# Optimization experiments

Measured on AMD Instinct MI355X. Metric: run time of the kernel, lower is better.

The kernel has to match this reference:

```python
import jax, jax.numpy as jnp
import numpy as np

N = 50000
E = 800000
EPS = 1e-5

def _gcn_conv(x, src, dst, norm, W, b):
    # PyG GCNConv: linear transform, normalized gather/scatter, then bias.
    xw = x @ W                                   # [N, out]
    msgs = xw[src] * norm[:, None]               # [E+N, out] gather
    out = jax.ops.segment_sum(msgs, dst, num_segments=N)  # scatter-add
    return out + b

def _bn_eval(x, gamma, beta, mean, var):
    return (x - mean) * jax.lax.rsqrt(var + EPS) * gamma + beta

def setup_inputs() -> dict:
    key = jax.random.key(0)
    ks = jax.random.split(key, 24)
    dims = [(128, 256), (256, 128), (128, 64), (64, 6)]
    inp = {
        "x": jax.random.normal(ks[0], (N, 128), dtype=jnp.float32),
        "edge_index": jax.random.randint(ks[1], (2, E), 0, N, dtype=jnp.int64),
    }
    i = 2
    for li, (fi, fo) in enumerate(dims, start=1):
        scale = 1.0 / np.sqrt(fi)
        inp[f"W{li}"] = jax.random.uniform(ks[i], (fi, fo), jnp.float32, -scale, scale); i += 1
        inp[f"b{li}"] = jnp.zeros((fo,), jnp.float32)
        if li < 4:  # BN after first three convs
            inp[f"g{li}"] = jnp.ones((fo,), jnp.float32)
            inp[f"be{li}"] = jnp.zeros((fo,), jnp.float32)
            inp[f"m{li}"] = 0.1 * jax.random.normal(ks[i], (fo,), jnp.float32); i += 1
            inp[f"v{li}"] = jax.random.uniform(ks[i], (fo,), jnp.float32, 0.5, 1.5); i += 1
    return inp

def reference(x, edge_index,
              W1, b1, g1, be1, m1, v1,
              W2, b2, g2, be2, m2, v2,
              W3, b3, g3, be3, m3, v3,
              W4, b4):
    # Add self-loops once; symmetric normalization deg^-1/2 (with self-loops).
    loops = jnp.arange(N, dtype=edge_index.dtype)
    src = jnp.concatenate([edge_index[0], loops])
    dst = jnp.concatenate([edge_index[1], loops])
    deg = jax.ops.segment_sum(jnp.ones_like(dst, dtype=x.dtype), dst, num_segments=N)
    dinv = jnp.where(deg > 0, jax.lax.rsqrt(deg), 0.0)
    norm = dinv[src] * dinv[dst]  # [E+N]

    h = _gcn_conv(x, src, dst, norm, W1, b1)
    h = jax.nn.relu(_bn_eval(h, g1, be1, m1, v1))  # dropout: no-op in eval
    h = _gcn_conv(h, src, dst, norm, W2, b2)
    h = jax.nn.relu(_bn_eval(h, g2, be2, m2, v2))
    h = _gcn_conv(h, src, dst, norm, W3, b3)
    h = jax.nn.relu(_bn_eval(h, g3, be3, m3, v3))
    return _gcn_conv(h, src, dst, norm, W4, b4)
```

## Files before the change

### kernel.cpp

```cpp
#include <hip/hip_runtime.h>
#include <hip/hip_bf16.h>
#include <hip/hip_fp16.h>

#define EPS 1e-5f

constexpr int NN = 50000;
constexpr int NE = 800000;

typedef __attribute__((ext_vector_type(8))) __bf16 bf16x8;
typedef __attribute__((ext_vector_type(4))) float f32x4;

__global__ void memset_i32(int* p, int n) {
  int i = blockIdx.x * blockDim.x + threadIdx.x;
  if (i < n) p[i] = 0;
}

__global__ void deg_kernel(const int* __restrict__ dst, int* __restrict__ degi, int n) {
  int i = blockIdx.x * blockDim.x + threadIdx.x;
  if (i < n) atomicAdd(&degi[dst[i]], 1);
}

__global__ __launch_bounds__(1024) void scan1(const int* __restrict__ cnt,
                                              int* __restrict__ incl,
                                              int* __restrict__ bsum, int n) {
  __shared__ int s[1024];
  int tid = threadIdx.x;
  int i = blockIdx.x * 1024 + tid;
  int v = (i < n) ? cnt[i] : 0;
  s[tid] = v;
  __syncthreads();
  for (int off = 1; off < 1024; off <<= 1) {
    int t = (tid >= off) ? s[tid - off] : 0;
    __syncthreads();
    s[tid] += t;
    __syncthreads();
  }
  if (i < n) incl[i] = s[tid];
  if (tid == 1023) bsum[blockIdx.x] = s[1023];
}

__global__ void scan2(int* __restrict__ bsum, int nb) {
  int lane = threadIdx.x;
  int v = (lane < nb) ? bsum[lane] : 0;
  int orig = v;
  for (int off = 1; off < 64; off <<= 1) {
    int t = __shfl_up(v, off, 64);
    if (lane >= off) v += t;
  }
  if (lane < nb) bsum[lane] = v - orig;
}

__global__ __launch_bounds__(1024) void scan3(const int* __restrict__ cnt,
                                              const int* __restrict__ incl,
                                              const int* __restrict__ bsum,
                                              int* __restrict__ rp,
                                              int* __restrict__ cursor,
                                              float* __restrict__ dinv, int n) {
  int tid = threadIdx.x;
  int i = blockIdx.x * 1024 + tid;
  if (i < n) {
    int v = incl[i] + bsum[blockIdx.x];
    rp[i + 1] = v;
    cursor[i] = v - cnt[i];
    dinv[i] = rsqrtf((float)(cnt[i] + 1));
  }
  if (i == 0) rp[0] = 0;
}

__global__ void fill_kernel(const int* __restrict__ src, const int* __restrict__ dst,
                            int* __restrict__ cursor, unsigned short* __restrict__ col,
                            int n) {
  int i = blockIdx.x * blockDim.x + threadIdx.x;
  if (i < n) {
    int pos = atomicAdd(&cursor[dst[i]], 1);
    col[pos] = (unsigned short)src[i];
  }
}

__device__ __forceinline__ void wsplit_one(const float* W, __bf16* th, __bf16* tl,
                                           int j, int K, int N) {
  int k = j / N, n = j - k * N;
  float v = W[j];
  __bf16 h = (__bf16)v;
  th[(size_t)n * K + k] = h;
  tl[(size_t)n * K + k] = (__bf16)(v - (float)h);
}

__global__ void wsplit_all(const float* __restrict__ W1, __bf16* t1h, __bf16* t1l,
                           const float* __restrict__ W2, __bf16* t2h, __bf16* t2l,
                           const float* __restrict__ W3, __bf16* t3h, __bf16* t3l,
                           const float* __restrict__ W4, __bf16* t4h, __bf16* t4l) {
  int i = blockIdx.x * blockDim.x + threadIdx.x;
  if (i < 32768) wsplit_one(W1, t1h, t1l, i, 128, 256);
  else if (i < 65536) wsplit_one(W2, t2h, t2l, i - 32768, 256, 128);
  else if (i < 73728) wsplit_one(W3, t3h, t3l, i - 65536, 128, 64);
  else if (i < 74112) wsplit_one(W4, t4h, t4l, i - 73728, 64, 6);
}

__global__ void scale_half(const float* __restrict__ x, const float* __restrict__ dinv,
                           __half* __restrict__ o, int n4) {
  int i = blockIdx.x * blockDim.x + threadIdx.x;
  if (i >= n4) return;
  int v = i >> 5;
  float4 t = ((const float4*)x)[i];
  float s = dinv[v];
  __half2 a = __floats2half2_rn(t.x * s, t.y * s);
  __half2 b = __floats2half2_rn(t.z * s, t.w * s);
  __half2* o2 = (__half2*)o;
  o2[i * 2] = a;
  o2[i * 2 + 1] = b;
}

template <int F, int EPI>
__global__ __launch_bounds__(256, 8) void prop_half(
    const __half* __restrict__ in, const int* __restrict__ rp,
    const unsigned short* __restrict__ col,
    const float* __restrict__ dinv, const float* __restrict__ bias,
    const float* __restrict__ gam, const float* __restrict__ bet,
    const float* __restrict__ mean, const float* __restrict__ var,
    __bf16* __restrict__ out_hi, __bf16* __restrict__ out_lo, int nnodes) {
  int tid = threadIdx.x;
  int wid = tid >> 6, lane = tid & 63;
  constexpr int VEC = F / 64;
  int v = blockIdx.x * 4 + wid;
  if (v >= nnodes) return;
  int e0 = rp[v], e1 = rp[v + 1];
  float acc[VEC];
  if constexpr (VEC == 2) {
    float2 f = __half22float2(*(const __half2*)(in + (size_t)v * F + lane * 2));
    acc[0] = f.x; acc[1] = f.y;
  } else {
    acc[0] = __half2float(in[(size_t)v * F + lane]);
  }
  int e1m1 = e1 - 1;
  constexpr int D = 8;
  for (int e = e0; e < e1; e += D) {
    int ss[D];
    float w[D];
    bool full = (e + D <= e1);
    if (full) {
#pragma unroll
      for (int u = 0; u < D; u++) { ss[u] = col[e + u]; w[u] = 1.f; }
    } else {
#pragma unroll
      for (int u = 0; u < D; u++) {
        int ei = e + u;
        ss[u] = col[ei < e1m1 ? ei : e1m1];
        w[u] = (ei < e1) ? 1.f : 0.f;
      }
    }
    if constexpr (VEC == 2) {
      __half2 hv[D];
#pragma unroll
      for (int u = 0; u < D; u++)
        hv[u] = *(const __half2*)(in + (size_t)ss[u] * F + lane * 2);
#pragma unroll
      for (int u = 0; u < D; u++) {
        float2 f = __half22float2(hv[u]);
        acc[0] = fmaf(f.x, w[u], acc[0]);
        acc[1] = fmaf(f.y, w[u], acc[1]);
      }
    } else {
      __half hv[D];
#pragma unroll
      for (int u = 0; u < D; u++) hv[u] = in[(size_t)ss[u] * F + lane];
#pragma unroll
      for (int u = 0; u < D; u++) acc[0] = fmaf(__half2float(hv[u]), w[u], acc[0]);
    }
  }
  float dv = dinv[v];
#pragma unroll
  for (int j = 0; j < VEC; j++) {
    int f = lane * VEC + j;
    float t = acc[j] * dv;
    if constexpr (EPI >= 1) {
      t += bias[f];
      t = (t - mean[f]) * rsqrtf(var[f] + EPS) * gam[f] + bet[f];
      t = fmaxf(t, 0.f);
    }
    __bf16 h = (__bf16)t;
    out_hi[(size_t)v * F + f] = h;
    out_lo[(size_t)v * F + f] = (__bf16)(t - (float)h);
  }
}

__global__ __launch_bounds__(256, 8) void prop_small(
    const float* __restrict__ in, const int* __restrict__ rp,
    const unsigned short* __restrict__ col,
    const float* __restrict__ dinv, const float* __restrict__ bias,
    float* __restrict__ out, int nnodes) {
  constexpr int F = 6;
  int tid = threadIdx.x;
  int wid = tid >> 6, lane = tid & 63;
  int g = lane >> 3, f = lane & 7;
  int v = (blockIdx.x * 4 + wid) * 8 + g;
  if (v >= nnodes || f >= F) return;
  int e0 = rp[v], e1 = rp[v + 1];
  float acc = in[(size_t)v * F + f];
  int e1m1 = e1 - 1;
  constexpr int D = 8;
  for (int e = e0; e < e1; e += D) {
    int ss[D];
    float w[D];
#pragma unroll
    for (int u = 0; u < D; u++) {
      int ei = e + u;
      ss[u] = col[ei < e1m1 ? ei : e1m1];
      w[u] = (ei < e1) ? 1.0f : 0.0f;
    }
#pragma unroll
    for (int u = 0; u < D; u++) acc = fmaf(in[(size_t)ss[u] * F + f], w[u], acc);
  }
  out[(size_t)v * F + f] = acc * dinv[v] + bias[f];
}

template <int BN, int EPI>
__global__ __launch_bounds__(256, 4) void mfma_gemm(
    const __bf16* __restrict__ Ahi, const __bf16* __restrict__ Alo,
    const __bf16* __restrict__ Bhi, const __bf16* __restrict__ Blo,
    const float* __restrict__ bias, const float* __restrict__ gam,
    const float* __restrict__ bet, const float* __restrict__ mean,
    const float* __restrict__ var, const float* __restrict__ dinv,
    float* __restrict__ Cf, __half* __restrict__ Ch,
    __bf16* __restrict__ Chi, __bf16* __restrict__ Clo,
    int M, int K, int N) {
  constexpr int BM = 128, BK = 32, NB = BN / 16;
  __shared__ __bf16 Ah[BM][BK + 8], Al[BM][BK + 8];
  __shared__ __bf16 Bh[BN][BK + 8], Bl[BN][BK + 8];
  int tid = threadIdx.x;
  int wid = tid >> 6, lane = tid & 63;
  int lr = lane & 15, lg = lane >> 4;
  int bm = blockIdx.x * BM, bn = blockIdx.y * BN;
  f32x4 acc[2][NB] = {};
  for (int k0 = 0; k0 < K; k0 += BK) {
#pragma unroll
    for (int c = 0; c < 2; c++) {
      int idx = tid + c * 256;
      int r = idx >> 2, s = idx & 3;
      int rg = bm + r;
      uint4 vh = {0, 0, 0, 0}, vl = {0, 0, 0, 0};
      if (rg < M) {
        size_t go = (size_t)rg * K + k0 + s * 8;
        vh = *reinterpret_cast<const uint4*>(Ahi + go);
        vl = *reinterpret_cast<const uint4*>(Alo + go);
      }
      *reinterpret_cast<uint4*>(&Ah[r][s * 8]) = vh;
      *reinterpret_cast<uint4*>(&Al[r][s * 8]) = vl;
    }
#pragma unroll
    for (int c = 0; c < (BN * 4 + 255) / 256; c++) {
      int idx = tid + c * 256;
      if (idx < BN * 4) {
        int r = idx >> 2, s = idx & 3;
        int rg = bn + r;
        uint4 vh = {0, 0, 0, 0}, vl = {0, 0, 0, 0};
        if (rg < N) {
          size_t go = (size_t)rg * K + k0 + s * 8;
          vh = *reinterpret_cast<const uint4*>(Bhi + go);
          vl = *reinterpret_cast<const uint4*>(Blo + go);
        }
        *reinterpret_cast<uint4*>(&Bh[r][s * 8]) = vh;
        *reinterpret_cast<uint4*>(&Bl[r][s * 8]) = vl;
      }
    }
    __syncthreads();
    int ar = wid * 32 + lr;
    bf16x8 ah0 = *reinterpret_cast<const bf16x8*>(&Ah[ar][lg * 8]);
    bf16x8 ah1 = *reinterpret_cast<const bf16x8*>(&Ah[ar + 16][lg * 8]);
    bf16x8 al0 = *reinterpret_cast<const bf16x8*>(&Al[ar][lg * 8]);
    bf16x8 al1 = *reinterpret_cast<const bf16x8*>(&Al[ar + 16][lg * 8]);
#pragma unroll
    for (int n = 0; n < NB; n++) {
      bf16x8 bh = *reinterpret_cast<const bf16x8*>(&Bh[n * 16 + lr][lg * 8]);
      bf16x8 bl = *reinterpret_cast<const bf16x8*>(&Bl[n * 16 + lr][lg * 8]);
      acc[0][n] = __builtin_amdgcn_mfma_f32_16x16x32_bf16(ah0, bh, acc[0][n], 0, 0, 0);
      acc[1][n] = __builtin_amdgcn_mfma_f32_16x16x32_bf16(ah1, bh, acc[1][n], 0, 0, 0);
      acc[0][n] = __builtin_amdgcn_mfma_f32_16x16x32_bf16(ah0, bl, acc[0][n], 0, 0, 0);
      acc[1][n] = __builtin_amdgcn_mfma_f32_16x16x32_bf16(ah1, bl, acc[1][n], 0, 0, 0);
      acc[0][n] = __builtin_amdgcn_mfma_f32_16x16x32_bf16(al0, bh, acc[0][n], 0, 0, 0);
      acc[1][n] = __builtin_amdgcn_mfma_f32_16x16x32_bf16(al1, bh, acc[1][n], 0, 0, 0);
    }
    __syncthreads();
  }
#pragma unroll
  for (int m = 0; m < 2; m++) {
    int row0 = bm + wid * 32 + m * 16 + lg * 4;
#pragma unroll
    for (int n = 0; n < NB; n++) {
      int colg = bn + n * 16 + lr;
#pragma unroll
      for (int r = 0; r < 4; r++) {
        int row = row0 + r;
        if (row >= M) continue;
        float t = acc[m][n][r];
        if constexpr (EPI == 0) {
          t += bias[colg];
          t = (t - mean[colg]) * rsqrtf(var[colg] + EPS) * gam[colg] + bet[colg];
          t = fmaxf(t, 0.f);
          __bf16 h = (__bf16)t;
          Chi[(size_t)row * N + colg] = h;
          Clo[(size_t)row * N + colg] = (__bf16)(t - (float)h);
        } else if constexpr (EPI == 1) {
          Ch[(size_t)row * N + colg] = __float2half(t * dinv[row]);
        } else {
          if (colg < N) Cf[(size_t)row * N + colg] = t * dinv[row];
        }
      }
    }
  }
}

extern "C" void kernel_launch(void* const* d_in, const int* in_sizes, int n_in,
                              void* d_out, int out_size, void* d_ws, size_t ws_size,
                              hipStream_t stream) {
  const float* x = (const float*)d_in[0];
  const int* ei = (const int*)d_in[1];
  const int* esrc = ei;
  const int* edst = ei + NE;
  const float* W1 = (const float*)d_in[2];  const float* b1 = (const float*)d_in[3];
  const float* g1 = (const float*)d_in[4];  const float* be1 = (const float*)d_in[5];
  const float* m1 = (const float*)d_in[6];  const float* v1 = (const float*)d_in[7];
  const float* W2 = (const float*)d_in[8];  const float* b2 = (const float*)d_in[9];
  const float* g2 = (const float*)d_in[10]; const float* be2 = (const float*)d_in[11];
  const float* m2 = (const float*)d_in[12]; const float* v2 = (const float*)d_in[13];
  const float* W3 = (const float*)d_in[14]; const float* b3 = (const float*)d_in[15];
  const float* g3 = (const float*)d_in[16]; const float* be3 = (const float*)d_in[17];
  const float* m3 = (const float*)d_in[18]; const float* v3 = (const float*)d_in[19];
  const float* W4 = (const float*)d_in[20]; const float* b4 = (const float*)d_in[21];
  float* out = (float*)d_out;

  char* base = (char*)d_ws;
  size_t off = 0;
  auto alloc = [&](size_t bytes) {
    void* p = base + off;
    off = (off + bytes + 255) & ~(size_t)255;
    return p;
  };
  __half* Xh = (__half*)alloc((size_t)NN * 128 * 2);
  float* F1 = (float*)alloc((size_t)NN * 6 * 4);
  __bf16* PAh = (__bf16*)alloc((size_t)NN * 128 * 2);
  __bf16* PAl = (__bf16*)alloc((size_t)NN * 128 * 2);
  __bf16* PHh = (__bf16*)alloc((size_t)NN * 256 * 2);
  __bf16* PHl = (__bf16*)alloc((size_t)NN * 256 * 2);
  __bf16* Wt1h = (__bf16*)alloc(128 * 256 * 2); __bf16* Wt1l = (__bf16*)alloc(128 * 256 * 2);
  __bf16* Wt2h = (__bf16*)alloc(256 * 128 * 2); __bf16* Wt2l = (__bf16*)alloc(256 * 128 * 2);
  __bf16* Wt3h = (__bf16*)alloc(128 * 64 * 2);  __bf16* Wt3l = (__bf16*)alloc(128 * 64 * 2);
  __bf16* Wt4h = (__bf16*)alloc(64 * 6 * 2);    __bf16* Wt4l = (__bf16*)alloc(64 * 6 * 2);
  int* degi = (int*)alloc((size_t)NN * 4);
  float* dinv = (float*)alloc((size_t)NN * 4);
  int* rp = (int*)alloc((size_t)(NN + 1) * 4);
  int* cursor = (int*)alloc((size_t)NN * 4);
  int* incl = (int*)alloc((size_t)NN * 4);
  int* bsum = (int*)alloc(64 * 4);
  unsigned short* col = (unsigned short*)alloc((size_t)NE * 2);

  const int nBlkN = (NN + 255) / 256;
  const int nBlkE = (NE + 255) / 256;
  const int nBlkScan = (NN + 1023) / 1024;
  const int gM = (NN + 127) / 128;
  const int gP = (NN + 3) / 4;

  memset_i32<<<nBlkN, 256, 0, stream>>>(degi, NN);
  deg_kernel<<<nBlkE, 256, 0, stream>>>(edst, degi, NE);
  scan1<<<nBlkScan, 1024, 0, stream>>>(degi, incl, bsum, NN);
  scan2<<<1, 64, 0, stream>>>(bsum, nBlkScan);
  scan3<<<nBlkScan, 1024, 0, stream>>>(degi, incl, bsum, rp, cursor, dinv, NN);
  fill_kernel<<<nBlkE, 256, 0, stream>>>(esrc, edst, cursor, col, NE);

  wsplit_all<<<(74112 + 255) / 256, 256, 0, stream>>>(W1, Wt1h, Wt1l, W2, Wt2h, Wt2l,
                                                      W3, Wt3h, Wt3l, W4, Wt4h, Wt4l);

  scale_half<<<(NN * 32 + 255) / 256, 256, 0, stream>>>(x, dinv, Xh, NN * 32);
  prop_half<128, 0><<<gP, 256, 0, stream>>>(Xh, rp, col, dinv, nullptr, nullptr, nullptr,
                                            nullptr, nullptr, PAh, PAl, NN);
  {
    dim3 g(gM, 2);
    mfma_gemm<128, 0><<<g, 256, 0, stream>>>(PAh, PAl, Wt1h, Wt1l, b1, g1, be1, m1, v1,
                                             nullptr, nullptr, nullptr, PHh, PHl,
                                             NN, 128, 256);
  }
  {
    dim3 g(gM, 1);
    mfma_gemm<128, 1><<<g, 256, 0, stream>>>(PHh, PHl, Wt2h, Wt2l, nullptr, nullptr,
                                             nullptr, nullptr, nullptr, dinv,
                                             nullptr, Xh, nullptr, nullptr, NN, 256, 128);
  }
  prop_half<128, 1><<<gP, 256, 0, stream>>>(Xh, rp, col, dinv, b2, g2, be2, m2, v2,
                                            PAh, PAl, NN);
  {
    dim3 g(gM, 1);
    mfma_gemm<64, 1><<<g, 256, 0, stream>>>(PAh, PAl, Wt3h, Wt3l, nullptr, nullptr,
                                            nullptr, nullptr, nullptr, dinv,
                                            nullptr, Xh, nullptr, nullptr, NN, 128, 64);
  }
  prop_half<64, 1><<<gP, 256, 0, stream>>>(Xh, rp, col, dinv, b3, g3, be3, m3, v3,
                                           PHh, PHl, NN);
  {
    dim3 g(gM, 1);
    mfma_gemm<16, 2><<<g, 256, 0, stream>>>(PHh, PHl, Wt4h, Wt4l, nullptr, nullptr,
                                            nullptr, nullptr, nullptr, dinv,
                                            F1, nullptr, nullptr, nullptr, NN, 64, 6);
  }
  prop_small<<<(NN + 31) / 32, 256, 0, stream>>>(F1, rp, col, dinv, b4, out, NN);
}
```

Before: 287.6 us.

## Partition propagation features into 32-wide column slabs and precompute CSR slot positions

Stores the fp16 propagation input as 32-column slabs (slab-major, node-minor), so each block gathers neighbor rows from a single slab that is small enough to stay cached. Inside a wave, four edge slots of 16 lanes each process edges in parallel and are combined with shuffles. Block indices are interleaved so that blocks working on different slabs of the same nodes run close together in time. CSR construction now records each edge's slot from the degree atomic as a byte, which removes the cursor array and the second atomic pass, and the weight split is merged with the input scaling. This adds reduction overhead, and storing the slot in a byte assumes no node has more than 255 incoming edges.

Result: slower. 355.8 us (+23.7%).

```diff
diff --git a/kernel.cpp b/kernel.cpp
--- a/kernel.cpp
+++ b/kernel.cpp
@@ -8,16 +8,13 @@
 constexpr int NE = 800000;
 
 typedef __attribute__((ext_vector_type(8))) __bf16 bf16x8;
+typedef __attribute__((ext_vector_type(2))) __bf16 bf16x2;
 typedef __attribute__((ext_vector_type(4))) float f32x4;
 
-__global__ void memset_i32(int* p, int n) {
+__global__ void deg_pos(const int* __restrict__ dst, int* __restrict__ degi,
+                        unsigned char* __restrict__ pos8, int n) {
   int i = blockIdx.x * blockDim.x + threadIdx.x;
-  if (i < n) p[i] = 0;
-}
-
-__global__ void deg_kernel(const int* __restrict__ dst, int* __restrict__ degi, int n) {
-  int i = blockIdx.x * blockDim.x + threadIdx.x;
-  if (i < n) atomicAdd(&degi[dst[i]], 1);
+  if (i < n) pos8[i] = (unsigned char)atomicAdd(&degi[dst[i]], 1);
 }
 
 __global__ __launch_bounds__(1024) void scan1(const int* __restrict__ cnt,
@@ -54,27 +51,22 @@
                                               const int* __restrict__ incl,
                                               const int* __restrict__ bsum,
                                               int* __restrict__ rp,
-                                              int* __restrict__ cursor,
                                               float* __restrict__ dinv, int n) {
   int tid = threadIdx.x;
   int i = blockIdx.x * 1024 + tid;
   if (i < n) {
-    int v = incl[i] + bsum[blockIdx.x];
-    rp[i + 1] = v;
-    cursor[i] = v - cnt[i];
+    rp[i + 1] = incl[i] + bsum[blockIdx.x];
     dinv[i] = rsqrtf((float)(cnt[i] + 1));
   }
   if (i == 0) rp[0] = 0;
 }
 
 __global__ void fill_kernel(const int* __restrict__ src, const int* __restrict__ dst,
-                            int* __restrict__ cursor, unsigned short* __restrict__ col,
-                            int n) {
+                            const int* __restrict__ rp,
+                            const unsigned char* __restrict__ pos8,
+                            unsigned short* __restrict__ col, int n) {
   int i = blockIdx.x * blockDim.x + threadIdx.x;
-  if (i < n) {
-    int pos = atomicAdd(&cursor[dst[i]], 1);
-    col[pos] = (unsigned short)src[i];
-  }
+  if (i < n) col[rp[dst[i]] + pos8[i]] = (unsigned short)src[i];
 }
 
 __device__ __forceinline__ void wsplit_one(const float* W, __bf16* th, __bf16* tl,
@@ -86,101 +78,99 @@
   tl[(size_t)n * K + k] = (__bf16)(v - (float)h);
 }
 
-__global__ void wsplit_all(const float* __restrict__ W1, __bf16* t1h, __bf16* t1l,
-                           const float* __restrict__ W2, __bf16* t2h, __bf16* t2l,
-                           const float* __restrict__ W3, __bf16* t3h, __bf16* t3l,
-                           const float* __restrict__ W4, __bf16* t4h, __bf16* t4l) {
+__global__ void wsplit_scale(const float* __restrict__ W1, __bf16* t1h, __bf16* t1l,
+                             const float* __restrict__ W2, __bf16* t2h, __bf16* t2l,
+                             const float* __restrict__ W3, __bf16* t3h, __bf16* t3l,
+                             const float* __restrict__ W4, __bf16* t4h, __bf16* t4l,
+                             const float* __restrict__ x, const float* __restrict__ dinv,
+                             __half* __restrict__ Xq) {
   int i = blockIdx.x * blockDim.x + threadIdx.x;
-  if (i < 32768) wsplit_one(W1, t1h, t1l, i, 128, 256);
-  else if (i < 65536) wsplit_one(W2, t2h, t2l, i - 32768, 256, 128);
-  else if (i < 73728) wsplit_one(W3, t3h, t3l, i - 65536, 128, 64);
-  else if (i < 74112) wsplit_one(W4, t4h, t4l, i - 73728, 64, 6);
-}
-
-__global__ void scale_half(const float* __restrict__ x, const float* __restrict__ dinv,
-                           __half* __restrict__ o, int n4) {
-  int i = blockIdx.x * blockDim.x + threadIdx.x;
-  if (i >= n4) return;
-  int v = i >> 5;
-  float4 t = ((const float4*)x)[i];
+  if (i < 32768) { wsplit_one(W1, t1h, t1l, i, 128, 256); return; }
+  if (i < 65536) { wsplit_one(W2, t2h, t2l, i - 32768, 256, 128); return; }
+  if (i < 73728) { wsplit_one(W3, t3h, t3l, i - 65536, 128, 64); return; }
+  if (i < 74112) { wsplit_one(W4, t4h, t4l, i - 73728, 64, 6); return; }
+  int k = i - 74112;
+  if (k >= NN * 32) return;
+  int v = k >> 5, f = (k & 31) * 4;
+  int q = f >> 5, off = f & 31;
+  float4 t = ((const float4*)x)[k];
   float s = dinv[v];
   __half2 a = __floats2half2_rn(t.x * s, t.y * s);
   __half2 b = __floats2half2_rn(t.z * s, t.w * s);
-  __half2* o2 = (__half2*)o;
-  o2[i * 2] = a;
-  o2[i * 2 + 1] = b;
+  __half2* d = (__half2*)(Xq + ((size_t)q * NN + v) * 32 + off);
+  d[0] = a;
+  d[1] = b;
 }
 
 template <int F, int EPI>
-__global__ __launch_bounds__(256, 8) void prop_half(
-    const __half* __restrict__ in, const int* __restrict__ rp,
+__global__ __launch_bounds__(256, 8) void prop_q(
+    const __half* __restrict__ Xq, const int* __restrict__ rp,
     const unsigned short* __restrict__ col,
     const float* __restrict__ dinv, const float* __restrict__ bias,
     const float* __restrict__ gam, const float* __restrict__ bet,
     const float* __restrict__ mean, const float* __restrict__ var,
     __bf16* __restrict__ out_hi, __bf16* __restrict__ out_lo, int nnodes) {
-  int tid = threadIdx.x;
-  int wid = tid >> 6, lane = tid & 63;
-  constexpr int VEC = F / 64;
-  int v = blockIdx.x * 4 + wid;
+  constexpr int NQ = F / 32;
+  int bid = blockIdx.x;
+  int q, gi;
+  if constexpr (NQ == 4) {
+    q = (bid & 7) >> 1;
+    gi = (bid >> 3) * 2 + (bid & 1);
+  } else {
+    q = (bid & 7) >> 2;
+    gi = (bid >> 3) * 4 + (bid & 3);
+  }
+  int tid = threadIdx.x, wid = tid >> 6, lane = tid & 63;
+  int j = lane & 15, slot = lane >> 4;
+  int v = gi * 4 + wid;
   if (v >= nnodes) return;
+  const __half* X = Xq + (size_t)q * nnodes * 32;
   int e0 = rp[v], e1 = rp[v + 1];
-  float acc[VEC];
-  if constexpr (VEC == 2) {
-    float2 f = __half22float2(*(const __half2*)(in + (size_t)v * F + lane * 2));
-    acc[0] = f.x; acc[1] = f.y;
-  } else {
-    acc[0] = __half2float(in[(size_t)v * F + lane]);
+  float ax = 0.f, ay = 0.f;
+  if (slot == 0) {
+    float2 s = __half22float2(*(const __half2*)(X + (size_t)v * 32 + j * 2));
+    ax = s.x;
+    ay = s.y;
   }
   int e1m1 = e1 - 1;
-  constexpr int D = 8;
-  for (int e = e0; e < e1; e += D) {
-    int ss[D];
-    float w[D];
-    bool full = (e + D <= e1);
-    if (full) {
-#pragma unroll
-      for (int u = 0; u < D; u++) { ss[u] = col[e + u]; w[u] = 1.f; }
-    } else {
-#pragma unroll
-      for (int u = 0; u < D; u++) {
-        int ei = e + u;
-        ss[u] = col[ei < e1m1 ? ei : e1m1];
-        w[u] = (ei < e1) ? 1.f : 0.f;
-      }
-    }
-    if constexpr (VEC == 2) {
-      __half2 hv[D];
-#pragma unroll
-      for (int u = 0; u < D; u++)
-        hv[u] = *(const __half2*)(in + (size_t)ss[u] * F + lane * 2);
-#pragma unroll
-      for (int u = 0; u < D; u++) {
-        float2 f = __half22float2(hv[u]);
-        acc[0] = fmaf(f.x, w[u], acc[0]);
-        acc[1] = fmaf(f.y, w[u], acc[1]);
-      }
-    } else {
-      __half hv[D];
-#pragma unroll
-      for (int u = 0; u < D; u++) hv[u] = in[(size_t)ss[u] * F + lane];
-#pragma unroll
-      for (int u = 0; u < D; u++) acc[0] = fmaf(__half2float(hv[u]), w[u], acc[0]);
-    }
-  }
-  float dv = dinv[v];
-#pragma unroll
-  for (int j = 0; j < VEC; j++) {
-    int f = lane * VEC + j;
-    float t = acc[j] * dv;
+  for (int e = e0; e < e1; e += 16) {
+    int ss[4];
+    float w[4];
+#pragma unroll
+    for (int u = 0; u < 4; u++) {
+      int ei = e + u * 4 + slot;
+      ss[u] = col[ei < e1 ? ei : e1m1];
+      w[u] = (ei < e1) ? 1.f : 0.f;
+    }
+    float2 fv[4];
+#pragma unroll
+    for (int u = 0; u < 4; u++)
+      fv[u] = __half22float2(*(const __half2*)(X + (size_t)ss[u] * 32 + j * 2));
+#pragma unroll
+    for (int u = 0; u < 4; u++) {
+      ax = fmaf(fv[u].x, w[u], ax);
+      ay = fmaf(fv[u].y, w[u], ay);
+    }
+  }
+  ax += __shfl_xor(ax, 16); ax += __shfl_xor(ax, 32);
+  ay += __shfl_xor(ay, 16); ay += __shfl_xor(ay, 32);
+  if (slot == 0) {
+    float dv = dinv[v];
+    int f0 = q * 32 + j * 2;
+    float t0 = ax * dv, t1 = ay * dv;
     if constexpr (EPI >= 1) {
-      t += bias[f];
-      t = (t - mean[f]) * rsqrtf(var[f] + EPS) * gam[f] + bet[f];
-      t = fmaxf(t, 0.f);
-    }
-    __bf16 h = (__bf16)t;
-    out_hi[(size_t)v * F + f] = h;
-    out_lo[(size_t)v * F + f] = (__bf16)(t - (float)h);
+      t0 += bias[f0];
+      t0 = (t0 - mean[f0]) * rsqrtf(var[f0] + EPS) * gam[f0] + bet[f0];
+      t0 = fmaxf(t0, 0.f);
+      t1 += bias[f0 + 1];
+      t1 = (t1 - mean[f0 + 1]) * rsqrtf(var[f0 + 1] + EPS) * gam[f0 + 1] + bet[f0 + 1];
+      t1 = fmaxf(t1, 0.f);
+    }
+    __bf16 h0 = (__bf16)t0, h1 = (__bf16)t1;
+    bf16x2 hv = {h0, h1};
+    bf16x2 lv = {(__bf16)(t0 - (float)h0), (__bf16)(t1 - (float)h1)};
+    *(bf16x2*)(out_hi + (size_t)v * F + f0) = hv;
+    *(bf16x2*)(out_lo + (size_t)v * F + f0) = lv;
   }
 }
 
@@ -301,7 +291,8 @@
           Chi[(size_t)row * N + colg] = h;
           Clo[(size_t)row * N + colg] = (__bf16)(t - (float)h);
         } else if constexpr (EPI == 1) {
-          Ch[(size_t)row * N + colg] = __float2half(t * dinv[row]);
+          int q = colg >> 5, offq = colg & 31;
+          Ch[((size_t)q * M + row) * 32 + offq] = __float2half(t * dinv[row]);
         } else {
           if (colg < N) Cf[(size_t)row * N + colg] = t * dinv[row];
         }
@@ -336,7 +327,7 @@
     off = (off + bytes + 255) & ~(size_t)255;
     return p;
   };
-  __half* Xh = (__half*)alloc((size_t)NN * 128 * 2);
+  __half* Xq = (__half*)alloc((size_t)NN * 128 * 2);
   float* F1 = (float*)alloc((size_t)NN * 6 * 4);
   __bf16* PAh = (__bf16*)alloc((size_t)NN * 128 * 2);
   __bf16* PAl = (__bf16*)alloc((size_t)NN * 128 * 2);
@@ -349,30 +340,27 @@
   int* degi = (int*)alloc((size_t)NN * 4);
   float* dinv = (float*)alloc((size_t)NN * 4);
   int* rp = (int*)alloc((size_t)(NN + 1) * 4);
-  int* cursor = (int*)alloc((size_t)NN * 4);
   int* incl = (int*)alloc((size_t)NN * 4);
   int* bsum = (int*)alloc(64 * 4);
   unsigned short* col = (unsigned short*)alloc((size_t)NE * 2);
-
-  const int nBlkN = (NN + 255) / 256;
+  unsigned char* pos8 = (unsigned char*)alloc((size_t)NE);
+
   const int nBlkE = (NE + 255) / 256;
   const int nBlkScan = (NN + 1023) / 1024;
   const int gM = (NN + 127) / 128;
-  const int gP = (NN + 3) / 4;
-
-  memset_i32<<<nBlkN, 256, 0, stream>>>(degi, NN);
-  deg_kernel<<<nBlkE, 256, 0, stream>>>(edst, degi, NE);
+
+  hipMemsetAsync(degi, 0, (size_t)NN * 4, stream);
+  deg_pos<<<nBlkE, 256, 0, stream>>>(edst, degi, pos8, NE);
   scan1<<<nBlkScan, 1024, 0, stream>>>(degi, incl, bsum, NN);
   scan2<<<1, 64, 0, stream>>>(bsum, nBlkScan);
-  scan3<<<nBlkScan, 1024, 0, stream>>>(degi, incl, bsum, rp, cursor, dinv, NN);
-  fill_kernel<<<nBlkE, 256, 0, stream>>>(esrc, edst, cursor, col, NE);
-
-  wsplit_all<<<(74112 + 255) / 256, 256, 0, stream>>>(W1, Wt1h, Wt1l, W2, Wt2h, Wt2l,
-                                                      W3, Wt3h, Wt3l, W4, Wt4h, Wt4l);
-
-  scale_half<<<(NN * 32 + 255) / 256, 256, 0, stream>>>(x, dinv, Xh, NN * 32);
-  prop_half<128, 0><<<gP, 256, 0, stream>>>(Xh, rp, col, dinv, nullptr, nullptr, nullptr,
-                                            nullptr, nullptr, PAh, PAl, NN);
+  scan3<<<nBlkScan, 1024, 0, stream>>>(degi, incl, bsum, rp, dinv, NN);
+  fill_kernel<<<nBlkE, 256, 0, stream>>>(esrc, edst, rp, pos8, col, NE);
+
+  wsplit_scale<<<(74112 + NN * 32 + 255) / 256, 256, 0, stream>>>(
+      W1, Wt1h, Wt1l, W2, Wt2h, Wt2l, W3, Wt3h, Wt3l, W4, Wt4h, Wt4l, x, dinv, Xq);
+
+  prop_q<128, 0><<<(NN / 4) * 8, 256, 0, stream>>>(Xq, rp, col, dinv, nullptr, nullptr,
+                                                   nullptr, nullptr, nullptr, PAh, PAl, NN);
   {
     dim3 g(gM, 2);
     mfma_gemm<128, 0><<<g, 256, 0, stream>>>(PAh, PAl, Wt1h, Wt1l, b1, g1, be1, m1, v1,
@@ -383,18 +371,18 @@
     dim3 g(gM, 1);
     mfma_gemm<128, 1><<<g, 256, 0, stream>>>(PHh, PHl, Wt2h, Wt2l, nullptr, nullptr,
                                              nullptr, nullptr, nullptr, dinv,
-                                             nullptr, Xh, nullptr, nullptr, NN, 256, 128);
-  }
-  prop_half<128, 1><<<gP, 256, 0, stream>>>(Xh, rp, col, dinv, b2, g2, be2, m2, v2,
-                                            PAh, PAl, NN);
+                                             nullptr, Xq, nullptr, nullptr, NN, 256, 128);
+  }
+  prop_q<128, 1><<<(NN / 4) * 8, 256, 0, stream>>>(Xq, rp, col, dinv, b2, g2, be2, m2, v2,
+                                                   PAh, PAl, NN);
   {
     dim3 g(gM, 1);
     mfma_gemm<64, 1><<<g, 256, 0, stream>>>(PAh, PAl, Wt3h, Wt3l, nullptr, nullptr,
                                             nullptr, nullptr, nullptr, dinv,
-                                            nullptr, Xh, nullptr, nullptr, NN, 128, 64);
-  }
-  prop_half<64, 1><<<gP, 256, 0, stream>>>(Xh, rp, col, dinv, b3, g3, be3, m3, v3,
-                                           PHh, PHl, NN);
+                                            nullptr, Xq, nullptr, nullptr, NN, 128, 64);
+  }
+  prop_q<64, 1><<<(NN / 4) * 4, 256, 0, stream>>>(Xq, rp, col, dinv, b3, g3, be3, m3, v3,
+                                                  PHh, PHl, NN);
   {
     dim3 g(gM, 1);
     mfma_gemm<16, 2><<<g, 256, 0, stream>>>(PHh, PHl, Wt4h, Wt4l, nullptr, nullptr,
```
